# Kernel optimization log

Hardware: AMD Instinct MI355X
Metric: run time of the kernel (lower is better)

Reference implementation:

```python
import jax, jax.numpy as jnp
import numpy as np

B, LQ, LKV, D, H = 4, 1024, 2048, 1024, 16
HD = D // H
EPS = 1e-5
NEG = -1e9


def _layernorm(x, w, b):
    mu = jnp.mean(x, axis=-1, keepdims=True)
    var = jnp.mean(jnp.square(x - mu), axis=-1, keepdims=True)
    return (x - mu) * jax.lax.rsqrt(var + EPS) * w + b


def setup_inputs() -> dict:
    key = jax.random.key(0)
    ks = jax.random.split(key, 10)
    q = jax.random.normal(ks[0], (B, LQ, D), dtype=jnp.float32)
    kv = jax.random.normal(ks[1], (B, LKV, D), dtype=jnp.float32)
    # ragged kv lengths; mask True == padding
    lengths = jax.random.randint(ks[2], (B,), LKV // 4, LKV + 1)
    mask = jnp.arange(LKV)[None, :] >= lengths[:, None]  # [B, LKV] bool
    s = 1.0 / np.sqrt(D)
    params = dict(
        norm_q_w=jnp.ones((D,), jnp.float32),
        norm_q_b=jnp.zeros((D,), jnp.float32),
        norm_kv_w=jnp.ones((D,), jnp.float32),
        norm_kv_b=jnp.zeros((D,), jnp.float32),
        Wq=jax.random.normal(ks[3], (D, D), jnp.float32) * s,
        bq=jnp.zeros((D,), jnp.float32),
        Wkv=jax.random.normal(ks[4], (2 * D, D), jnp.float32) * s,
        bkv=jnp.zeros((2 * D,), jnp.float32),
        Wo=jax.random.normal(ks[5], (D, D), jnp.float32) * s,
        bo=jnp.zeros((D,), jnp.float32),
    )
    return dict(q=q, kv=kv, mask=mask, **params)


def reference(q, kv, mask, norm_q_w, norm_q_b, norm_kv_w, norm_kv_b, Wq, bq, Wkv, bkv, Wo, bo):
    q_res = q
    qn = _layernorm(q, norm_q_w, norm_q_b)
    kvn = _layernorm(kv, norm_kv_w, norm_kv_b)
    # projections
    qh = (qn @ Wq.T + bq).reshape(B, LQ, H, HD)
    kvp = (kvn @ Wkv.T + bkv).reshape(B, LKV, 2, H, HD)
    k, v = kvp[:, :, 0], kvp[:, :, 1]  # [B, LKV, H, HD]
    # masked cross attention (math-equivalent to varlen flash attn over unpadded kv)
    scale = 1.0 / np.sqrt(HD)
    scores = jnp.einsum('bqhd,bkhd->bhqk', qh, k) * scale
    scores = jnp.where(mask[:, None, None, :], NEG, scores)
    attn = jax.nn.softmax(scores, axis=-1)
    out = jnp.einsum('bhqk,bkhd->bqhd', attn, v).reshape(B, LQ, D)
    # out proj + residual (dropout is identity in eval)
    return q_res + (out @ Wo.T + bo)


if __name__ == '__main__':
    inp = setup_inputs()
    y = reference(**inp)
    print(y.shape, y.dtype)
```

## Files before the change

kernel.cpp:

```cpp
#include <hip/hip_runtime.h>

#define DEV __device__ __forceinline__

typedef unsigned short u16;
typedef float  floatx4 __attribute__((ext_vector_type(4)));
typedef unsigned int uintx2 __attribute__((ext_vector_type(2)));
typedef unsigned int uintx4 __attribute__((ext_vector_type(4)));
typedef __bf16 bf16x8 __attribute__((ext_vector_type(8)));

constexpr int cB = 4, cLQ = 1024, cLKV = 2048, cD = 1024, cH = 16, cHD = 64;

DEV u16 f2bf(float f) {
  unsigned u = __builtin_bit_cast(unsigned, f);
  u += 0x7fffu + ((u >> 16) & 1u);
  return (u16)(u >> 16);
}

DEV bf16x8 ld_frag(const u16* p) {
  uintx4 u = *(const uintx4*)p;
  return __builtin_bit_cast(bf16x8, u);
}

DEV floatx4 mfma16(bf16x8 a, bf16x8 b, floatx4 c) {
  return __builtin_amdgcn_mfma_f32_16x16x32_bf16(a, b, c, 0, 0, 0);
}

DEV float ex2(float x) { return __builtin_amdgcn_exp2f(x); }

DEV unsigned pkbf(float a, float b) {
  return (__builtin_bit_cast(unsigned, b) & 0xffff0000u) |
         (__builtin_bit_cast(unsigned, a) >> 16);
}

DEV void pl32(unsigned &a, unsigned &b) {
#if __has_builtin(__builtin_amdgcn_permlane32_swap)
  uintx2 r = __builtin_amdgcn_permlane32_swap(a, b, false, false);
  a = r[0]; b = r[1];
#else
  asm("v_permlane32_swap_b32 %0, %1" : "+v"(a), "+v"(b));
#endif
}
DEV void pl16(unsigned &a, unsigned &b) {
#if __has_builtin(__builtin_amdgcn_permlane16_swap)
  uintx2 r = __builtin_amdgcn_permlane16_swap(a, b, false, false);
  a = r[0]; b = r[1];
#else
  asm("v_permlane16_swap_b32 %0, %1" : "+v"(a), "+v"(b));
#endif
}

__global__ __launch_bounds__(256) void prep_kernel(
    const float* __restrict__ q, const float* __restrict__ kv,
    const float* __restrict__ nqw, const float* __restrict__ nqb,
    const float* __restrict__ nkw, const float* __restrict__ nkb,
    u16* __restrict__ qn, u16* __restrict__ kvn,
    const float* __restrict__ Wq, const float* __restrict__ Wkv,
    const float* __restrict__ Wo, u16* __restrict__ wqb,
    u16* __restrict__ wkvb, u16* __restrict__ wob,
    const void* __restrict__ mask, int* __restrict__ lens) {
  int bid = blockIdx.x, tid = threadIdx.x;
  if (bid < cB * (cLQ + cLKV)) {
    const float* x; const float* w; const float* b; u16* dst;
    if (bid < cB * cLQ) {
      x = q + (size_t)bid * cD; w = nqw; b = nqb; dst = qn + (size_t)bid * cD;
    } else {
      int r2 = bid - cB * cLQ;
      x = kv + (size_t)r2 * cD; w = nkw; b = nkb; dst = kvn + (size_t)r2 * cD;
    }
    float4 v = ((const float4*)x)[tid];
    __shared__ float sbuf[8];
    float s = v.x + v.y + v.z + v.w;
    #pragma unroll
    for (int m = 1; m < 64; m <<= 1) s += __shfl_xor(s, m, 64);
    if ((tid & 63) == 0) sbuf[tid >> 6] = s;
    __syncthreads();
    float mean = (sbuf[0] + sbuf[1] + sbuf[2] + sbuf[3]) * (1.f / cD);
    float dx = v.x - mean, dy = v.y - mean, dz = v.z - mean, dw = v.w - mean;
    float ss = dx * dx + dy * dy + dz * dz + dw * dw;
    #pragma unroll
    for (int m = 1; m < 64; m <<= 1) ss += __shfl_xor(ss, m, 64);
    if ((tid & 63) == 0) sbuf[4 + (tid >> 6)] = ss;
    __syncthreads();
    float var = (sbuf[4] + sbuf[5] + sbuf[6] + sbuf[7]) * (1.f / cD);
    float rs = rsqrtf(var + 1e-5f);
    float4 wv = ((const float4*)w)[tid];
    float4 bv = ((const float4*)b)[tid];
    ushort4 o;
    o.x = f2bf(dx * rs * wv.x + bv.x);
    o.y = f2bf(dy * rs * wv.y + bv.y);
    o.z = f2bf(dz * rs * wv.z + bv.z);
    o.w = f2bf(dw * rs * wv.w + bv.w);
    ((ushort4*)dst)[tid] = o;
  } else if (bid < cB * (cLQ + cLKV) + 4096) {
    int gi = (bid - cB * (cLQ + cLKV)) * 256 + tid;
    const float* src; u16* dst; int off;
    if (gi < 262144)      { src = Wq;  dst = wqb;  off = gi; }
    else if (gi < 786432) { src = Wkv; dst = wkvb; off = gi - 262144; }
    else                  { src = Wo;  dst = wob;  off = gi - 786432; }
    float4 v = ((const float4*)src)[off];
    ushort4 o;
    o.x = f2bf(v.x); o.y = f2bf(v.y); o.z = f2bf(v.z); o.w = f2bf(v.w);
    ((ushort4*)dst)[off] = o;
  } else {
    __shared__ int smode;
    __shared__ int cnt[cB];
    if (tid == 0) smode = 0;
    if (tid < cB) cnt[tid] = 0;
    __syncthreads();
    const unsigned* mi = (const unsigned*)mask;
    int bad = 0;
    for (int i = tid; i < cB * cLKV / 4; i += 256)
      if (mi[i] > 1u) bad = 1;
    if (bad) smode = 1;
    __syncthreads();
    if (smode == 0) {
      for (int b = 0; b < cB; b++) {
        int c = 0;
        for (int i = tid; i < cLKV; i += 256) c += (mi[(size_t)b * cLKV + i] == 0u);
        atomicAdd(&cnt[b], c);
      }
    } else {
      const unsigned char* m8 = (const unsigned char*)mask;
      for (int b = 0; b < cB; b++) {
        int c = 0;
        for (int i = tid; i < cLKV; i += 256) c += (m8[(size_t)b * cLKV + i] == 0);
        atomicAdd(&cnt[b], c);
      }
    }
    __syncthreads();
    if (tid < cB) lens[tid] = cnt[tid];
    if (tid == 0) {
      int ord[4] = {0, 1, 2, 3};
      #pragma unroll
      for (int a = 0; a < 3; a++)
        #pragma unroll
        for (int d = 0; d < 3; d++)
          if (cnt[ord[d]] < cnt[ord[d + 1]]) {
            int tswap = ord[d]; ord[d] = ord[d + 1]; ord[d + 1] = tswap;
          }
      #pragma unroll
      for (int a = 0; a < 4; a++) lens[4 + a] = ord[a];
    }
  }
}

struct TileCtx {
  int m16, quad, wr, wc;
};

DEV void gemm_mainloop(const u16* __restrict__ A, const u16* __restrict__ Bm,
                       int row0, int col0, int K, u16* As, u16* Bs,
                       const TileCtx& t, floatx4 (&acc)[4][4]) {
  int tid = threadIdx.x;
  int wave = tid >> 6, lane = tid & 63;
  int srow = wave * 16 + (lane >> 2);
  int sseg = (lane & 3) * 8;
  const u16* ga = A + (size_t)(row0 + srow) * K + sseg;
  const u16* gb = Bm + (size_t)(col0 + srow) * K + sseg;
  const size_t rstep = (size_t)64 * K;
  int woff = srow * 32 + sseg;

  uintx4 a0 = *(const uintx4*)ga;
  uintx4 a1 = *(const uintx4*)(ga + rstep);
  uintx4 b0 = *(const uintx4*)gb;
  uintx4 b1 = *(const uintx4*)(gb + rstep);
  *(uintx4*)(As + woff) = a0;
  *(uintx4*)(As + woff + 2048) = a1;
  *(uintx4*)(Bs + woff) = b0;
  *(uintx4*)(Bs + woff + 2048) = b1;
  a0 = *(const uintx4*)(ga + 32);
  a1 = *(const uintx4*)(ga + rstep + 32);
  b0 = *(const uintx4*)(gb + 32);
  b1 = *(const uintx4*)(gb + rstep + 32);
  __syncthreads();

  for (int k0 = 0; k0 < K; k0 += 32) {
    int cur = (k0 >> 5) & 1;
    const u16* rA = As + cur * 4096;
    const u16* rB = Bs + cur * 4096;
    bf16x8 af[4], bfr[4];
    #pragma unroll
    for (int i = 0; i < 4; i++)
      af[i] = ld_frag(&rA[(t.wr * 64 + i * 16 + t.m16) * 32 + t.quad * 8]);
    #pragma unroll
    for (int j = 0; j < 4; j++)
      bfr[j] = ld_frag(&rB[(t.wc * 64 + j * 16 + t.m16) * 32 + t.quad * 8]);
    if (k0 + 32 < K) {
      u16* nA = As + (cur ^ 1) * 4096 + woff;
      u16* nB = Bs + (cur ^ 1) * 4096 + woff;
      *(uintx4*)nA = a0;
      *(uintx4*)(nA + 2048) = a1;
      *(uintx4*)nB = b0;
      *(uintx4*)(nB + 2048) = b1;
      if (k0 + 64 < K) {
        a0 = *(const uintx4*)(ga + k0 + 64);
        a1 = *(const uintx4*)(ga + rstep + k0 + 64);
        b0 = *(const uintx4*)(gb + k0 + 64);
        b1 = *(const uintx4*)(gb + rstep + k0 + 64);
      }
    }
    #pragma unroll
    for (int i = 0; i < 4; i++)
      #pragma unroll
      for (int j = 0; j < 4; j++)
        acc[i][j] = mfma16(af[i], bfr[j], acc[i][j]);
    __syncthreads();
  }
}

__global__ __launch_bounds__(256) void proj_fused(
    const u16* __restrict__ qn, const u16* __restrict__ wqb,
    const float* __restrict__ bq, u16* __restrict__ qhb,
    const u16* __restrict__ kvn, const u16* __restrict__ wkvb,
    const float* __restrict__ bkv, u16* __restrict__ khb,
    u16* __restrict__ vthb, const int* __restrict__ lens) {
  __shared__ __align__(16) u16 As[2 * 128 * 32];
  __shared__ __align__(16) u16 Bs[2 * 128 * 32];
  int bid = blockIdx.x;
  int lane = threadIdx.x & 63;
  TileCtx t;
  t.m16 = lane & 15; t.quad = lane >> 4;
  int wave = threadIdx.x >> 6;
  t.wr = wave >> 1; t.wc = wave & 1;

  bool isQ = bid < 256;
  int row0, col0;
  const u16* A; const u16* Bm; const float* bias;
  if (isQ) {
    row0 = (bid >> 3) * 128; col0 = (bid & 7) * 128;
    A = qn; Bm = wqb; bias = bq;
  } else {
    int b2 = bid - 256;
    row0 = (b2 >> 4) * 128; col0 = (b2 & 15) * 128;
    A = kvn; Bm = wkvb; bias = bkv;
    if ((row0 & (cLKV - 1)) >= lens[row0 >> 11]) return;
  }

  floatx4 z = {0.f, 0.f, 0.f, 0.f};
  floatx4 acc[4][4];
  #pragma unroll
  for (int i = 0; i < 4; i++)
    #pragma unroll
    for (int j = 0; j < 4; j++) acc[i][j] = z;

  gemm_mainloop(A, Bm, row0, col0, cD, As, Bs, t, acc);

  #pragma unroll
  for (int j = 0; j < 4; j++) {
    int col = col0 + t.wc * 64 + j * 16 + t.m16;
    float bs = bias[col];
    if (isQ) {
      #pragma unroll
      for (int i = 0; i < 4; i++) {
        int crow = row0 + t.wr * 64 + i * 16 + t.quad * 4;
        #pragma unroll
        for (int r = 0; r < 4; r++)
          qhb[(size_t)(crow + r) * cD + col] =
              f2bf((acc[i][j][r] + bs) * 0.18033688f);
      }
    } else {
      bool isK = col < cD;
      int c2 = isK ? col : col - cD;
      int hh = c2 >> 6, dd = c2 & 63;
      #pragma unroll
      for (int i = 0; i < 4; i++) {
        int crow = row0 + t.wr * 64 + i * 16 + t.quad * 4;
        int bb = crow >> 11, kvp = crow & (cLKV - 1);
        if (isK) {
          u16* dst = khb + ((size_t)(bb * cH + hh) * cLKV + kvp) * 64 + dd;
          #pragma unroll
          for (int r = 0; r < 4; r++) dst[(size_t)r * 64] = f2bf(acc[i][j][r] + bs);
        } else {
          u16* dst = vthb + ((size_t)(bb * cH + hh) * 64 + dd) * cLKV + kvp;
          ushort4 o;
          o.x = f2bf(acc[i][j][0] + bs);
          o.y = f2bf(acc[i][j][1] + bs);
          o.z = f2bf(acc[i][j][2] + bs);
          o.w = f2bf(acc[i][j][3] + bs);
          *(ushort4*)dst = o;
        }
      }
    }
  }
}

__global__ __launch_bounds__(256) void gemm_o(
    const u16* __restrict__ A, const u16* __restrict__ Bm,
    const float* __restrict__ bias, const float* __restrict__ res,
    float* __restrict__ Cout, int N, int K) {
  __shared__ __align__(16) u16 As[2 * 128 * 32];
  __shared__ __align__(16) u16 Bs[2 * 128 * 32];
  int bid0 = blockIdx.x;
  int swz = (bid0 & 7) * 32 + (bid0 >> 3);
  int row0 = (swz >> 3) * 128, col0 = (swz & 7) * 128;
  int lane = threadIdx.x & 63;
  TileCtx t;
  t.m16 = lane & 15; t.quad = lane >> 4;
  int wave = threadIdx.x >> 6;
  t.wr = wave >> 1; t.wc = wave & 1;

  floatx4 z = {0.f, 0.f, 0.f, 0.f};
  floatx4 acc[4][4];
  #pragma unroll
  for (int i = 0; i < 4; i++)
    #pragma unroll
    for (int j = 0; j < 4; j++) acc[i][j] = z;

  gemm_mainloop(A, Bm, row0, col0, K, As, Bs, t, acc);

  #pragma unroll
  for (int j = 0; j < 4; j++) {
    int col = col0 + t.wc * 64 + j * 16 + t.m16;
    float bs = bias[col];
    #pragma unroll
    for (int i = 0; i < 4; i++) {
      int crow = row0 + t.wr * 64 + i * 16 + t.quad * 4;
      #pragma unroll
      for (int r = 0; r < 4; r++) {
        size_t idx = (size_t)(crow + r) * N + col;
        Cout[idx] = acc[i][j][r] + bs + res[idx];
      }
    }
  }
}

constexpr int KS = 72;

template<bool MASK>
DEV void attn_compute(int k0, int len, const u16* __restrict__ Kt,
                      const u16* __restrict__ Vt,
                      const bf16x8 (&qf)[2][2], int m16, int quad,
                      float (&lsum)[2], floatx4 (&accO)[2][4]) {
  floatx4 z = {0.f, 0.f, 0.f, 0.f};
  bf16x8 kf[4][2];
  #pragma unroll
  for (int t = 0; t < 4; t++) {
    kf[t][0] = ld_frag(&Kt[(t * 16 + m16) * KS + quad * 8]);
    kf[t][1] = ld_frag(&Kt[(t * 16 + m16) * KS + 32 + quad * 8]);
  }
  floatx4 s[2][4];
  #pragma unroll
  for (int g = 0; g < 2; g++)
    #pragma unroll
    for (int t = 0; t < 4; t++) {
      floatx4 tt = z;
      tt = mfma16(kf[t][0], qf[g][0], tt);
      tt = mfma16(kf[t][1], qf[g][1], tt);
      s[g][t] = tt;
    }
  bf16x8 ap0[2], ap1[2];
  #pragma unroll
  for (int g = 0; g < 2; g++) {
    unsigned p[4][2];
    #pragma unroll
    for (int t = 0; t < 4; t++) {
      float e0, e1, e2, e3;
      if (MASK) {
        int key = k0 + t * 16 + quad * 4;
        e0 = (key     < len) ? ex2(s[g][t][0]) : 0.f;
        e1 = (key + 1 < len) ? ex2(s[g][t][1]) : 0.f;
        e2 = (key + 2 < len) ? ex2(s[g][t][2]) : 0.f;
        e3 = (key + 3 < len) ? ex2(s[g][t][3]) : 0.f;
      } else {
        e0 = ex2(s[g][t][0]);
        e1 = ex2(s[g][t][1]);
        e2 = ex2(s[g][t][2]);
        e3 = ex2(s[g][t][3]);
      }
      lsum[g] += (e0 + e1) + (e2 + e3);
      p[t][0] = pkbf(e0, e1);
      p[t][1] = pkbf(e2, e3);
    }
    unsigned a0 = p[0][0], b0 = p[1][0]; pl32(a0, b0); pl16(a0, b0);
    unsigned a1 = p[0][1], b1 = p[1][1]; pl32(a1, b1); pl16(a1, b1);
    uintx4 lo = {a0, a1, b0, b1};
    unsigned c0 = p[2][0], d0 = p[3][0]; pl32(c0, d0); pl16(c0, d0);
    unsigned c1 = p[2][1], d1 = p[3][1]; pl32(c1, d1); pl16(c1, d1);
    uintx4 hi = {c0, c1, d0, d1};
    ap0[g] = __builtin_bit_cast(bf16x8, lo);
    ap1[g] = __builtin_bit_cast(bf16x8, hi);
  }
  #pragma unroll
  for (int db = 0; db < 4; db++) {
    bf16x8 bv0 = ld_frag(&Vt[(db * 16 + m16) * KS + quad * 8]);
    bf16x8 bv1 = ld_frag(&Vt[(db * 16 + m16) * KS + 32 + quad * 8]);
    #pragma unroll
    for (int g = 0; g < 2; g++) {
      accO[g][db] = mfma16(ap0[g], bv0, accO[g][db]);
      accO[g][db] = mfma16(ap1[g], bv1, accO[g][db]);
    }
  }
}

__global__ __launch_bounds__(256) void attn_kernel(
    const u16* __restrict__ qh, const u16* __restrict__ kh,
    const u16* __restrict__ vth, const int* __restrict__ lens,
    u16* __restrict__ out) {
  int bid = blockIdx.x;
  int r = bid >> 7;
  int rank = r ^ (r >> 1);
  int b = lens[4 + rank];
  int combo = bid & 127;
  int h = combo >> 3;
  int qt = combo & 7;
  int len = lens[b];
  int wave = threadIdx.x >> 6, lane = threadIdx.x & 63;
  int m16 = lane & 15, quad = lane >> 4;

  __shared__ __align__(16) u16 Kt[64 * KS];
  __shared__ __align__(16) u16 Vt[64 * KS];

  int q0 = qt * 128 + wave * 32;
  const u16* qp = qh + ((size_t)(b * cLQ + q0 + m16) * cH + h) * cHD;
  bf16x8 qf[2][2];
  qf[0][0] = ld_frag(qp + quad * 8);
  qf[0][1] = ld_frag(qp + 32 + quad * 8);
  qf[1][0] = ld_frag(qp + (size_t)16 * cD + quad * 8);
  qf[1][1] = ld_frag(qp + (size_t)16 * cD + 32 + quad * 8);

  const u16* kbase = kh + (size_t)(b * cH + h) * cLKV * cHD;
  const u16* vbase = vth + (size_t)(b * cH + h) * cHD * cLKV;

  int srow = threadIdx.x >> 3;
  int sseg = threadIdx.x & 7;
  const u16* kg = kbase + (size_t)srow * cHD + sseg * 8;
  const u16* vg = vbase + (size_t)srow * cLKV + sseg * 8;

  float lsum[2] = {0.f, 0.f};
  floatx4 z = {0.f, 0.f, 0.f, 0.f};
  floatx4 accO[2][4] = {{z, z, z, z}, {z, z, z, z}};

  int nch = (len + 63) >> 6;
  uintx4 ka  = *(const uintx4*)kg;
  uintx4 kb2 = *(const uintx4*)(kg + (size_t)32 * cHD);
  uintx4 va  = *(const uintx4*)vg;
  uintx4 vb  = *(const uintx4*)(vg + (size_t)32 * cLKV);

  for (int c = 0; c < nch; c++) {
    int k0 = c * 64;
    __syncthreads();
    *(uintx4*)&Kt[srow * KS + sseg * 8] = ka;
    *(uintx4*)&Kt[(srow + 32) * KS + sseg * 8] = kb2;
    *(uintx4*)&Vt[srow * KS + sseg * 8] = va;
    *(uintx4*)&Vt[(srow + 32) * KS + sseg * 8] = vb;
    if (c + 1 < nch) {
      int kn = k0 + 64;
      ka  = *(const uintx4*)(kg + (size_t)kn * cHD);
      kb2 = *(const uintx4*)(kg + (size_t)(kn + 32) * cHD);
      va  = *(const uintx4*)(vg + kn);
      vb  = *(const uintx4*)(vg + (size_t)32 * cLKV + kn);
    }
    __syncthreads();
    if (k0 + 64 <= len)
      attn_compute<false>(k0, len, Kt, Vt, qf, m16, quad, lsum, accO);
    else
      attn_compute<true>(k0, len, Kt, Vt, qf, m16, quad, lsum, accO);
  }

  #pragma unroll
  for (int g = 0; g < 2; g++) {
    float tsum = lsum[g];
    tsum += __shfl_xor(tsum, 16, 64);
    tsum += __shfl_xor(tsum, 32, 64);
    #pragma unroll
    for (int rr = 0; rr < 4; rr++) {
      float inv = 1.0f / __shfl(tsum, quad * 4 + rr, 16);
      int qg = q0 + g * 16 + quad * 4 + rr;
      size_t base = ((size_t)(b * cLQ + qg) * cH + h) * cHD;
      #pragma unroll
      for (int db = 0; db < 4; db++)
        out[base + db * 16 + m16] = f2bf(accO[g][db][rr] * inv);
    }
  }
}

extern "C" void kernel_launch(void* const* d_in, const int* in_sizes, int n_in,
                              void* d_out, int out_size, void* d_ws, size_t ws_size,
                              hipStream_t stream) {
  const float* q    = (const float*)d_in[0];
  const float* kv   = (const float*)d_in[1];
  const void*  mask = d_in[2];
  const float* nqw  = (const float*)d_in[3];
  const float* nqb  = (const float*)d_in[4];
  const float* nkw  = (const float*)d_in[5];
  const float* nkb  = (const float*)d_in[6];
  const float* Wq   = (const float*)d_in[7];
  const float* bq   = (const float*)d_in[8];
  const float* Wkv  = (const float*)d_in[9];
  const float* bkv  = (const float*)d_in[10];
  const float* Wo   = (const float*)d_in[11];
  const float* bo   = (const float*)d_in[12];
  float* out = (float*)d_out;

  char* w = (char*)d_ws;
  int* lens = (int*)w;       w += 256;
  u16* qn   = (u16*)w;       w += (size_t)cB * cLQ * cD * 2;
  u16* kvn  = (u16*)w;       w += (size_t)cB * cLKV * cD * 2;
  u16* wqb  = (u16*)w;       w += (size_t)cD * cD * 2;
  u16* wkvb = (u16*)w;       w += (size_t)2 * cD * cD * 2;
  u16* wob  = (u16*)w;       w += (size_t)cD * cD * 2;
  u16* qhb  = (u16*)w;       w += (size_t)cB * cLQ * cD * 2;
  u16* khb  = (u16*)w;       w += (size_t)cB * cH * cLKV * cHD * 2;
  u16* vthb = (u16*)w;       w += (size_t)cB * cH * cHD * cLKV * 2;
  u16* aob  = (u16*)w;

  prep_kernel<<<cB * (cLQ + cLKV) + 4096 + 1, 256, 0, stream>>>(
      q, kv, nqw, nqb, nkw, nkb, qn, kvn,
      Wq, Wkv, Wo, wqb, wkvb, wob, mask, lens);
  proj_fused<<<1280, 256, 0, stream>>>(
      qn, wqb, bq, qhb, kvn, wkvb, bkv, khb, vthb, lens);
  attn_kernel<<<512, 256, 0, stream>>>(
      qhb, khb, vthb, lens, aob);
  gemm_o<<<dim3(256), 256, 0, stream>>>(
      aob, wob, bo, q, out, cD, cD);
}
```

Baseline: 267.5 us.

## Use one wave per row in layernorm prep and smaller 64x128 output GEMM tiles

The layernorm part of prep now gives each 64-lane wave a whole row, so a block handles four rows and the shared-memory reductions and block barriers go away. Weight conversion is reorganised so each block converts four chunks, which cuts the prep grid from about 16k blocks to 4097. The output projection GEMM moves from 128x128 tiles on 256 blocks to 64x128 tiles on 512 blocks, with its own inline register-staged double-buffered main loop. The smaller tiles should fill the GPU better, at the cost of more re-reads of the B operand.

```diff
diff --git a/kernel.cpp b/kernel.cpp
--- a/kernel.cpp
+++ b/kernel.cpp
@@ -59,48 +59,63 @@
     u16* __restrict__ wkvb, u16* __restrict__ wob,
     const void* __restrict__ mask, int* __restrict__ lens) {
   int bid = blockIdx.x, tid = threadIdx.x;
-  if (bid < cB * (cLQ + cLKV)) {
+  if (bid < 3072) {
+    int row = bid * 4 + (tid >> 6);
+    int lane = tid & 63;
     const float* x; const float* w; const float* b; u16* dst;
-    if (bid < cB * cLQ) {
-      x = q + (size_t)bid * cD; w = nqw; b = nqb; dst = qn + (size_t)bid * cD;
+    if (row < cB * cLQ) {
+      x = q + (size_t)row * cD; w = nqw; b = nqb; dst = qn + (size_t)row * cD;
     } else {
-      int r2 = bid - cB * cLQ;
+      int r2 = row - cB * cLQ;
       x = kv + (size_t)r2 * cD; w = nkw; b = nkb; dst = kvn + (size_t)r2 * cD;
     }
-    float4 v = ((const float4*)x)[tid];
-    __shared__ float sbuf[8];
-    float s = v.x + v.y + v.z + v.w;
+    const float4* xf = (const float4*)x;
+    float4 v[4];
+    #pragma unroll
+    for (int c = 0; c < 4; c++) v[c] = xf[lane + 64 * c];
+    float s = 0.f;
+    #pragma unroll
+    for (int c = 0; c < 4; c++) s += (v[c].x + v[c].y) + (v[c].z + v[c].w);
     #pragma unroll
     for (int m = 1; m < 64; m <<= 1) s += __shfl_xor(s, m, 64);
-    if ((tid & 63) == 0) sbuf[tid >> 6] = s;
-    __syncthreads();
-    float mean = (sbuf[0] + sbuf[1] + sbuf[2] + sbuf[3]) * (1.f / cD);
-    float dx = v.x - mean, dy = v.y - mean, dz = v.z - mean, dw = v.w - mean;
-    float ss = dx * dx + dy * dy + dz * dz + dw * dw;
+    float mean = s * (1.f / cD);
+    float ss = 0.f;
+    #pragma unroll
+    for (int c = 0; c < 4; c++) {
+      v[c].x -= mean; v[c].y -= mean; v[c].z -= mean; v[c].w -= mean;
+      ss += (v[c].x * v[c].x + v[c].y * v[c].y) +
+            (v[c].z * v[c].z + v[c].w * v[c].w);
+    }
     #pragma unroll
     for (int m = 1; m < 64; m <<= 1) ss += __shfl_xor(ss, m, 64);
-    if ((tid & 63) == 0) sbuf[4 + (tid >> 6)] = ss;
-    __syncthreads();
-    float var = (sbuf[4] + sbuf[5] + sbuf[6] + sbuf[7]) * (1.f / cD);
-    float rs = rsqrtf(var + 1e-5f);
-    float4 wv = ((const float4*)w)[tid];
-    float4 bv = ((const float4*)b)[tid];
-    ushort4 o;
-    o.x = f2bf(dx * rs * wv.x + bv.x);
-    o.y = f2bf(dy * rs * wv.y + bv.y);
-    o.z = f2bf(dz * rs * wv.z + bv.z);
-    o.w = f2bf(dw * rs * wv.w + bv.w);
-    ((ushort4*)dst)[tid] = o;
-  } else if (bid < cB * (cLQ + cLKV) + 4096) {
-    int gi = (bid - cB * (cLQ + cLKV)) * 256 + tid;
-    const float* src; u16* dst; int off;
-    if (gi < 262144)      { src = Wq;  dst = wqb;  off = gi; }
-    else if (gi < 786432) { src = Wkv; dst = wkvb; off = gi - 262144; }
-    else                  { src = Wo;  dst = wob;  off = gi - 786432; }
-    float4 v = ((const float4*)src)[off];
-    ushort4 o;
-    o.x = f2bf(v.x); o.y = f2bf(v.y); o.z = f2bf(v.z); o.w = f2bf(v.w);
-    ((ushort4*)dst)[off] = o;
+    float rs = rsqrtf(ss * (1.f / cD) + 1e-5f);
+    const float4* wf = (const float4*)w;
+    const float4* bf = (const float4*)b;
+    #pragma unroll
+    for (int c = 0; c < 4; c++) {
+      float4 wv = wf[lane + 64 * c];
+      float4 bv = bf[lane + 64 * c];
+      ushort4 o;
+      o.x = f2bf(v[c].x * rs * wv.x + bv.x);
+      o.y = f2bf(v[c].y * rs * wv.y + bv.y);
+      o.z = f2bf(v[c].z * rs * wv.z + bv.z);
+      o.w = f2bf(v[c].w * rs * wv.w + bv.w);
+      ((ushort4*)dst)[lane + 64 * c] = o;
+    }
+  } else if (bid < 4096) {
+    int base = (bid - 3072) * 1024;
+    #pragma unroll
+    for (int c = 0; c < 4; c++) {
+      int gi = base + c * 256 + tid;
+      const float* src; u16* dst; int off;
+      if (gi < 262144)      { src = Wq;  dst = wqb;  off = gi; }
+      else if (gi < 786432) { src = Wkv; dst = wkvb; off = gi - 262144; }
+      else                  { src = Wo;  dst = wob;  off = gi - 786432; }
+      float4 v = ((const float4*)src)[off];
+      ushort4 o;
+      o.x = f2bf(v.x); o.y = f2bf(v.y); o.z = f2bf(v.z); o.w = f2bf(v.w);
+      ((ushort4*)dst)[off] = o;
+    }
   } else {
     __shared__ int smode;
     __shared__ int cnt[cB];
@@ -288,33 +303,78 @@
     const u16* __restrict__ A, const u16* __restrict__ Bm,
     const float* __restrict__ bias, const float* __restrict__ res,
     float* __restrict__ Cout, int N, int K) {
-  __shared__ __align__(16) u16 As[2 * 128 * 32];
+  __shared__ __align__(16) u16 As[2 * 64 * 32];
   __shared__ __align__(16) u16 Bs[2 * 128 * 32];
-  int bid0 = blockIdx.x;
-  int swz = (bid0 & 7) * 32 + (bid0 >> 3);
-  int row0 = (swz >> 3) * 128, col0 = (swz & 7) * 128;
   int lane = threadIdx.x & 63;
-  TileCtx t;
-  t.m16 = lane & 15; t.quad = lane >> 4;
+  int m16 = lane & 15, quad = lane >> 4;
   int wave = threadIdx.x >> 6;
-  t.wr = wave >> 1; t.wc = wave & 1;
+  int wr = wave >> 1, wc = wave & 1;
+  int row0 = blockIdx.y * 64, col0 = blockIdx.x * 128;
+
+  int tid = threadIdx.x;
+  int srow = tid >> 2;
+  int sseg = (tid & 3) * 8;
+  const u16* ga = A + (size_t)(row0 + srow) * K + sseg;
+  const u16* gb = Bm + (size_t)(col0 + srow) * K + sseg;
+  const size_t rstep = (size_t)64 * K;
+  int woff = srow * 32 + sseg;
+
+  uintx4 a0 = *(const uintx4*)ga;
+  uintx4 b0 = *(const uintx4*)gb;
+  uintx4 b1 = *(const uintx4*)(gb + rstep);
+  *(uintx4*)(As + woff) = a0;
+  *(uintx4*)(Bs + woff) = b0;
+  *(uintx4*)(Bs + woff + 2048) = b1;
+  a0 = *(const uintx4*)(ga + 32);
+  b0 = *(const uintx4*)(gb + 32);
+  b1 = *(const uintx4*)(gb + rstep + 32);
+  __syncthreads();
 
   floatx4 z = {0.f, 0.f, 0.f, 0.f};
-  floatx4 acc[4][4];
-  #pragma unroll
-  for (int i = 0; i < 4; i++)
+  floatx4 acc[2][4];
+  #pragma unroll
+  for (int i = 0; i < 2; i++)
     #pragma unroll
     for (int j = 0; j < 4; j++) acc[i][j] = z;
 
-  gemm_mainloop(A, Bm, row0, col0, K, As, Bs, t, acc);
+  for (int k0 = 0; k0 < K; k0 += 32) {
+    int cur = (k0 >> 5) & 1;
+    const u16* rA = As + cur * 2048;
+    const u16* rB = Bs + cur * 4096;
+    bf16x8 af[2], bfr[4];
+    #pragma unroll
+    for (int i = 0; i < 2; i++)
+      af[i] = ld_frag(&rA[(wr * 32 + i * 16 + m16) * 32 + quad * 8]);
+    #pragma unroll
+    for (int j = 0; j < 4; j++)
+      bfr[j] = ld_frag(&rB[(wc * 64 + j * 16 + m16) * 32 + quad * 8]);
+    if (k0 + 32 < K) {
+      u16* nA = As + (cur ^ 1) * 2048 + woff;
+      u16* nB = Bs + (cur ^ 1) * 4096 + woff;
+      *(uintx4*)nA = a0;
+      *(uintx4*)nB = b0;
+      *(uintx4*)(nB + 2048) = b1;
+      if (k0 + 64 < K) {
+        a0 = *(const uintx4*)(ga + k0 + 64);
+        b0 = *(const uintx4*)(gb + k0 + 64);
+        b1 = *(const uintx4*)(gb + rstep + k0 + 64);
+      }
+    }
+    #pragma unroll
+    for (int i = 0; i < 2; i++)
+      #pragma unroll
+      for (int j = 0; j < 4; j++)
+        acc[i][j] = mfma16(af[i], bfr[j], acc[i][j]);
+    __syncthreads();
+  }
 
   #pragma unroll
   for (int j = 0; j < 4; j++) {
-    int col = col0 + t.wc * 64 + j * 16 + t.m16;
+    int col = col0 + wc * 64 + j * 16 + m16;
     float bs = bias[col];
     #pragma unroll
-    for (int i = 0; i < 4; i++) {
-      int crow = row0 + t.wr * 64 + i * 16 + t.quad * 4;
+    for (int i = 0; i < 2; i++) {
+      int crow = row0 + wr * 32 + i * 16 + quad * 4;
       #pragma unroll
       for (int r = 0; r < 4; r++) {
         size_t idx = (size_t)(crow + r) * N + col;
@@ -504,13 +564,13 @@
   u16* vthb = (u16*)w;       w += (size_t)cB * cH * cHD * cLKV * 2;
   u16* aob  = (u16*)w;
 
-  prep_kernel<<<cB * (cLQ + cLKV) + 4096 + 1, 256, 0, stream>>>(
+  prep_kernel<<<4097, 256, 0, stream>>>(
       q, kv, nqw, nqb, nkw, nkb, qn, kvn,
       Wq, Wkv, Wo, wqb, wkvb, wob, mask, lens);
   proj_fused<<<1280, 256, 0, stream>>>(
       qn, wqb, bq, qhb, kvn, wkvb, bkv, khb, vthb, lens);
   attn_kernel<<<512, 256, 0, stream>>>(
       qhb, khb, vthb, lens, aob);
-  gemm_o<<<dim3(256), 256, 0, stream>>>(
+  gemm_o<<<dim3(cD / 128, cB * cLQ / 64), 256, 0, stream>>>(
       aob, wob, bo, q, out, cD, cD);
 }
```

After: 262.5 us. No clear change (-1.9%).
